# Kernel tuning notes

Measured on AMD Instinct MI355X. Metric: run time of the kernel, lower is better.

Reference implementation:

```python
import jax, jax.numpy as jnp
import numpy as np

P = 113          # vocab (modulus)
D = 128          # residual_dim
H = 4            # n_heads (hardcoded in Model)
DH = D // H      # head_dim = 32
HID = 4 * D      # mlp hidden = 512
BATCH = 131072
RATE = 0.5       # attention_rate


def setup_inputs() -> dict:
    key = jax.random.key(0)
    ks = jax.random.split(key, 12)
    std = 1.0 / D ** 0.5
    x = jax.random.randint(ks[0], (BATCH, 2), 0, P)
    tok_emb = jax.random.normal(ks[1], (P, D), jnp.float32) / D ** 0.5
    pos_emb = jax.random.normal(ks[2], (2, D), jnp.float32) / D ** 0.5
    W_Q = jax.random.normal(ks[3], (H, D, DH), jnp.float32) * std
    W_K = jax.random.normal(ks[4], (H, D, DH), jnp.float32) * std
    W_V = jax.random.normal(ks[5], (H, D, DH), jnp.float32) * std
    W_O = jax.random.normal(ks[6], (H, DH, D), jnp.float32) * std
    # nn.Linear default init: U(-1/sqrt(fan_in), 1/sqrt(fan_in))
    b1_bound = 1.0 / D ** 0.5
    W1 = jax.random.uniform(ks[7], (D, HID), jnp.float32, -b1_bound, b1_bound)
    b1 = jax.random.uniform(ks[8], (HID,), jnp.float32, -b1_bound, b1_bound)
    b2_bound = 1.0 / HID ** 0.5
    W2 = jax.random.uniform(ks[9], (HID, D), jnp.float32, -b2_bound, b2_bound)
    b2 = jax.random.uniform(ks[10], (D,), jnp.float32, -b2_bound, b2_bound)
    W_U = jax.random.normal(ks[11], (P, D), jnp.float32) / P ** 0.5
    return dict(x=x, tok_emb=tok_emb, pos_emb=pos_emb, W_Q=W_Q, W_K=W_K,
                W_V=W_V, W_O=W_O, W1=W1, b1=b1, W2=W2, b2=b2, W_U=W_U)


def reference(x, tok_emb, pos_emb, W_Q, W_K, W_V, W_O, W1, b1, W2, b2, W_U):
    # embed: [B,2,D]
    resid = tok_emb[x] + pos_emb[None, :, :]
    # attention
    q = jnp.einsum('bpd,hdk->bphk', resid, W_Q)
    k = jnp.einsum('bpd,hdk->bphk', resid, W_K)
    v = jnp.einsum('bpd,hdk->bphk', resid, W_V)
    scores = jnp.einsum('bqhk,bshk->bhqs', q, k) / DH ** 0.5  # [B,H,2,2]
    pattern = jax.nn.softmax(scores, axis=-1)
    pattern = (1.0 - RATE) + RATE * pattern  # uniform blend, no causal mask
    z = jnp.einsum('bshk,bhqs->bqhk', v, pattern)
    attn_out = jnp.einsum('bqhk,hkd->bqd', z, W_O)
    resid = resid + attn_out
    # mlp
    h = jax.nn.relu(resid @ W1 + b1)
    resid = resid + (h @ W2 + b2)
    # unembed: [B,2,P]
    logits = jnp.einsum('vd,bpd->bpv', W_U, resid)
    return logits
```

## Files before the change

### kernel.cpp

```cpp
#include <hip/hip_runtime.h>
#include <hip/hip_bf16.h>
#include <stdint.h>

typedef __hip_bfloat16 bf16;
typedef __attribute__((ext_vector_type(8))) short short8;
typedef __attribute__((ext_vector_type(4))) float float4v;

#define NVOCAB 113
#define NPAIR (113 * 113)
#define DDIM 128
#define HIDDIM 512
#define CAP 128
#define LDSB_CAP 1024

#define OFF_B1  145792
#define OFF_B2  211840

#define BOFF_WOT 0
#define BOFF_W1T 16384
#define BOFF_W2T (16384 + 65536)
#define BOFF_WUP (16384 + 65536 + 65536)
#define BTOTAL   (16384 + 65536 + 65536 + 16384)

__device__ __forceinline__ uint16_t f2b(float f) {
  bf16 h = __float2bfloat16(f);
  return *(uint16_t*)&h;
}
__device__ __forceinline__ float b2f(uint16_t u) {
  return __uint_as_float(((uint32_t)u) << 16);
}
__device__ __forceinline__ float ldsrc(const void* p, int i, int isb) {
  return isb ? b2f(((const uint16_t*)p)[i]) : ((const float*)p)[i];
}

struct SrcPtrs { const void* p[11]; };

__global__ void init_kernel(const uint32_t* __restrict__ tok_raw,
                            const uint32_t* __restrict__ x_raw,
                            int* __restrict__ flags,
                            int* __restrict__ cursor) {
  const int idx = blockIdx.x * 256 + threadIdx.x;
  for (int i = idx; i < NPAIR; i += gridDim.x * 256) cursor[i] = 0;
  if (blockIdx.x == 0) {
    __shared__ int cnt_bf16, cnt_xnz;
    if (threadIdx.x == 0) { cnt_bf16 = 0; cnt_xnz = 0; }
    __syncthreads();
    uint32_t u = tok_raw[threadIdx.x];
    int e = (u >> 7) & 0xff;
    if (e >= 100 && e <= 126) atomicAdd(&cnt_bf16, 1);
    uint32_t xv = x_raw[2 * threadIdx.x + 1];
    if (xv != 0u) atomicAdd(&cnt_xnz, 1);
    __syncthreads();
    if (threadIdx.x == 0) {
      flags[0] = (cnt_bf16 >= 128) ? 1 : 0;
      flags[1] = (cnt_xnz == 0) ? 1 : 0;
    }
  }
}

__global__ void __launch_bounds__(384) build_kernel(
    SrcPtrs sp, const uint32_t* __restrict__ x_raw,
    const int* __restrict__ flags, float* __restrict__ wf,
    float* __restrict__ resid_pre, float* __restrict__ qt,
    float* __restrict__ kt, float* __restrict__ vt,
    uint16_t* __restrict__ wb, int* __restrict__ cursor,
    int* __restrict__ blist, int B) {
  const int tid = threadIdx.x;
  const int blk = blockIdx.x;
  const int isb = flags[0];

  if (blk < 226) {
    const int row = blk;
    const int t = row >> 1, p = row & 1;
    __shared__ float r[DDIM];
    if (tid < DDIM) {
      float rv = ldsrc(sp.p[0], t * DDIM + tid, isb) +
                 ldsrc(sp.p[1], p * DDIM + tid, isb);
      r[tid] = rv;
      resid_pre[row * DDIM + tid] = rv;
    }
    __syncthreads();
    const int which = tid >> 7, jj = tid & 127;
    const int h = jj >> 5, j = jj & 31;
    const void* wsrc = sp.p[2 + which];
    const int base = h * 4096 + j;
    float a = 0.f;
    if (isb) {
      const uint16_t* w16 = (const uint16_t*)wsrc;
      #pragma unroll 8
      for (int d = 0; d < 128; ++d)
        a += r[d] * b2f(w16[base + d * 32]);
    } else {
      const float* w32 = (const float*)wsrc;
      #pragma unroll 8
      for (int d = 0; d < 128; ++d)
        a += r[d] * w32[base + d * 32];
    }
    float* outp = (which == 0) ? qt : (which == 1) ? kt : vt;
    outp[row * DDIM + jj] = a;
  } else if (blk < 653) {
    const int idx = (blk - 226) * 384 + tid;
    if (idx < BTOTAL) {
      float v;
      if (idx < BOFF_W1T) {
        int l = idx, d = l >> 7, c = l & 127;
        v = ldsrc(sp.p[5], c * 128 + d, isb);
      } else if (idx < BOFF_W2T) {
        int l = idx - BOFF_W1T, n = l >> 7, d = l & 127;
        v = ldsrc(sp.p[6], d * 512 + n, isb);
      } else if (idx < BOFF_WUP) {
        int l = idx - BOFF_W2T, d = l >> 9, j = l & 511;
        v = ldsrc(sp.p[8], j * 128 + d, isb);
      } else {
        int l = idx - BOFF_WUP, vv = l >> 7, d = l & 127;
        v = (vv < NVOCAB) ? ldsrc(sp.p[10], vv * 128 + d, isb) : 0.f;
      }
      wb[idx] = f2b(v);
    }
  } else if (blk < 655) {
    const int i = (blk - 653) * 384 + tid;
    if (i < 512) wf[OFF_B1 + i] = ldsrc(sp.p[7], i, isb);
    else if (i < 640) wf[OFF_B2 + (i - 512)] = ldsrc(sp.p[9], i - 512, isb);
  } else {
    const int is64 = flags[1];
    const int nthr = (gridDim.x - 655) * 384;
    for (int b = (blk - 655) * 384 + tid; b < B; b += nthr) {
      int t0, t1;
      if (is64) {
        t0 = (int)x_raw[4 * b];
        t1 = (int)x_raw[4 * b + 2];
      } else {
        t0 = (int)x_raw[2 * b];
        t1 = (int)x_raw[2 * b + 1];
      }
      t0 = min(max(t0, 0), NVOCAB - 1);
      t1 = min(max(t1, 0), NVOCAB - 1);
      const int pair = t0 * NVOCAB + t1;
      int pos = atomicAdd(&cursor[pair], 1);
      if (pos < CAP) blist[pair * CAP + pos] = b;
    }
  }
}

__global__ void __launch_bounds__(256, 4) pair_mfma_kernel(
    const float* __restrict__ resid_pre, const float* __restrict__ qt,
    const float* __restrict__ kt, const float* __restrict__ vt,
    const float* __restrict__ wf, const uint16_t* __restrict__ wb,
    const int* __restrict__ cursor, const int* __restrict__ blist,
    float* __restrict__ out) {
  __shared__ uint16_t bufH[16 * 512];
  __shared__ uint16_t bufZ[16 * 128];
  __shared__ uint16_t bufS[16 * 128];
  __shared__ float    spat[8 * 16];
  __shared__ int      smeta[8];
  __shared__ int      ldsb[LDSB_CAP];

  const int tid = threadIdx.x;
  const int blk = blockIdx.x;
  const int lane = tid & 63;
  const int npar = tid >> 6;
  const int l15 = lane & 15, quad = lane >> 4;
  const int mA = l15;

  #define ROW_OF(row_) ({                                        \
    int pr_ = blk * 8 + ((row_) >> 1);                           \
    if (pr_ >= NPAIR) pr_ = NPAIR - 1;                           \
    int t0_ = pr_ / NVOCAB, t1_ = pr_ - t0_ * NVOCAB;            \
    ((row_) & 1) ? t1_ * 2 + 1 : t0_ * 2; })

  if (tid < 8) {
    const int pr = blk * 8 + tid;
    smeta[tid] = (pr < NPAIR) ? min(cursor[pr], CAP) : 0;
  }
  float rpre[2][4];
  #pragma unroll
  for (int ni = 0; ni < 2; ++ni) {
    const int n = (npar + ni * 4) * 16 + l15;
    #pragma unroll
    for (int r = 0; r < 4; ++r)
      rpre[ni][r] = resid_pre[ROW_OF(quad * 4 + r) * DDIM + n];
  }
  float bias1v[8], bias2v[2];
  #pragma unroll
  for (int ni = 0; ni < 8; ++ni)
    bias1v[ni] = wf[OFF_B1 + (npar + ni * 4) * 16 + l15];
  #pragma unroll
  for (int ni = 0; ni < 2; ++ni)
    bias2v[ni] = wf[OFF_B2 + (npar + ni * 4) * 16 + l15];
  const int zm = tid >> 4, zc0 = (tid & 15) * 8;
  float4 zv0a, zv0b, zv1a, zv1b;
  {
    const int zr0 = ROW_OF((zm >> 1) * 2);
    const int zr1 = ROW_OF((zm >> 1) * 2 + 1);
    const float4* p0 = (const float4*)(vt + zr0 * DDIM + zc0);
    const float4* p1 = (const float4*)(vt + zr1 * DDIM + zc0);
    zv0a = p0[0]; zv0b = p0[1]; zv1a = p1[0]; zv1b = p1[1];
  }

  if (tid < 128) {
    const int pl = tid >> 4, s = tid & 15;
    const int pair = blk * 8 + pl;
    if (pair < NPAIR) {
      const int t0 = pair / NVOCAB, t1 = pair - t0 * NVOCAB;
      const int row0 = t0 * 2, row1 = t1 * 2 + 1;
      const int h = s >> 2, qp = (s >> 1) & 1, spp = s & 1;
      const float4* qrow = (const float4*)(qt + (qp ? row1 : row0) * DDIM + h * 32);
      const float4* krow = (const float4*)(kt + (spp ? row1 : row0) * DDIM + h * 32);
      float acc = 0.f;
      #pragma unroll
      for (int j = 0; j < 8; ++j) {
        float4 qv = qrow[j], kv = krow[j];
        acc += qv.x * kv.x + qv.y * kv.y + qv.z * kv.z + qv.w * kv.w;
      }
      spat[pl * 16 + s] = acc * 0.17677669529663687f;
    } else {
      spat[pl * 16 + s] = 0.f;
    }
  }
  __syncthreads();

  int sPre[9];
  sPre[0] = 0;
  #pragma unroll
  for (int q = 0; q < 8; ++q) sPre[q + 1] = sPre[q] + smeta[q];
  const int tot = sPre[8];

  if (tid < 64) {
    const int pl = tid >> 3, s = tid & 7;
    const int base = pl * 16 + s * 2;
    float s0 = spat[base], s1 = spat[base + 1];
    float m = fmaxf(s0, s1);
    float e0 = __expf(s0 - m), e1 = __expf(s1 - m);
    float inv = 1.f / (e0 + e1);
    spat[base]     = 0.5f + 0.5f * e0 * inv;
    spat[base + 1] = 0.5f + 0.5f * e1 * inv;
  } else {
    const int cap = (tot < LDSB_CAP) ? tot : LDSB_CAP;
    for (int i = tid - 64; i < cap; i += 192) {
      int q = 0;
      #pragma unroll
      for (int qq = 1; qq < 8; ++qq)
        if (i >= sPre[qq]) q = qq;
      ldsb[i] = blist[(blk * 8 + q) * CAP + (i - sPre[q])];
    }
  }
  __syncthreads();

  {
    const int pl = zm >> 1, qp = zm & 1;
    const int h = zc0 >> 5;
    const float p0 = spat[pl * 16 + h * 4 + qp * 2];
    const float p1 = spat[pl * 16 + h * 4 + qp * 2 + 1];
    float v0[8] = {zv0a.x, zv0a.y, zv0a.z, zv0a.w, zv0b.x, zv0b.y, zv0b.z, zv0b.w};
    float v1[8] = {zv1a.x, zv1a.y, zv1a.z, zv1a.w, zv1b.x, zv1b.y, zv1b.z, zv1b.w};
    short8 pk;
    #pragma unroll
    for (int e = 0; e < 8; ++e)
      pk[e] = (short)f2b(p0 * v0[e] + p1 * v1[e]);
    *(short8*)&bufZ[(zm * 16 + ((zc0 >> 3) ^ zm)) * 8] = pk;
  }
  __syncthreads();

  float smid[2][4];

  {
    short8 af[4];
    #pragma unroll
    for (int ks = 0; ks < 4; ++ks)
      af[ks] = *(const short8*)&bufZ[(mA * 16 + ((ks * 4 + quad) ^ mA)) * 8];
    short8 bW[2][4];
    #pragma unroll
    for (int ni = 0; ni < 2; ++ni) {
      const int n = (npar + ni * 4) * 16 + l15;
      const uint16_t* bp = wb + BOFF_WOT + n * 128 + quad * 8;
      #pragma unroll
      for (int ks = 0; ks < 4; ++ks)
        bW[ni][ks] = *(const short8*)(bp + ks * 32);
    }
    #pragma unroll
    for (int ni = 0; ni < 2; ++ni) {
      const int n = (npar + ni * 4) * 16 + l15;
      float4v acc = {0.f, 0.f, 0.f, 0.f};
      #pragma unroll
      for (int ks = 0; ks < 4; ++ks)
        acc = __builtin_amdgcn_mfma_f32_16x16x32_bf16(af[ks], bW[ni][ks], acc, 0, 0, 0);
      #pragma unroll
      for (int r = 0; r < 4; ++r) {
        const int row = quad * 4 + r;
        float v = acc[r] + rpre[ni][r];
        smid[ni][r] = v;
        bufS[(row * 16 + ((n >> 3) ^ row)) * 8 + (n & 7)] = f2b(v);
      }
    }
  }
  __syncthreads();

  {
    short8 af[4];
    #pragma unroll
    for (int ks = 0; ks < 4; ++ks)
      af[ks] = *(const short8*)&bufS[(mA * 16 + ((ks * 4 + quad) ^ mA)) * 8];
    #pragma unroll
    for (int half = 0; half < 2; ++half) {
      short8 bW[4][4];
      #pragma unroll
      for (int nj = 0; nj < 4; ++nj) {
        const int ni = half * 4 + nj;
        const int n = (npar + ni * 4) * 16 + l15;
        const uint16_t* bp = wb + BOFF_W1T + n * 128 + quad * 8;
        #pragma unroll
        for (int ks = 0; ks < 4; ++ks)
          bW[nj][ks] = *(const short8*)(bp + ks * 32);
      }
      #pragma unroll
      for (int nj = 0; nj < 4; ++nj) {
        const int ni = half * 4 + nj;
        const int n = (npar + ni * 4) * 16 + l15;
        float4v acc = {0.f, 0.f, 0.f, 0.f};
        #pragma unroll
        for (int ks = 0; ks < 4; ++ks)
          acc = __builtin_amdgcn_mfma_f32_16x16x32_bf16(af[ks], bW[nj][ks], acc, 0, 0, 0);
        const float bias = bias1v[ni];
        #pragma unroll
        for (int r = 0; r < 4; ++r) {
          const int row = quad * 4 + r;
          bufH[(row * 64 + ((n >> 3) ^ row)) * 8 + (n & 7)] =
              f2b(fmaxf(acc[r] + bias, 0.f));
        }
      }
    }
  }
  __syncthreads();

  {
    const int n0 = npar * 16 + l15;
    const int n1 = (npar + 4) * 16 + l15;
    const uint16_t* bp0 = wb + BOFF_W2T + n0 * 512 + quad * 8;
    const uint16_t* bp1 = wb + BOFF_W2T + n1 * 512 + quad * 8;
    float4v acc0 = {0.f, 0.f, 0.f, 0.f};
    float4v acc1 = {0.f, 0.f, 0.f, 0.f};
    #pragma unroll
    for (int half = 0; half < 2; ++half) {
      short8 ah[8], b0[8], b1[8];
      #pragma unroll
      for (int k8 = 0; k8 < 8; ++k8) {
        const int ks = half * 8 + k8;
        ah[k8] = *(const short8*)&bufH[(mA * 64 + ((ks * 4 + quad) ^ mA)) * 8];
        b0[k8] = *(const short8*)(bp0 + ks * 32);
        b1[k8] = *(const short8*)(bp1 + ks * 32);
      }
      #pragma unroll
      for (int k8 = 0; k8 < 8; ++k8) {
        acc0 = __builtin_amdgcn_mfma_f32_16x16x32_bf16(ah[k8], b0[k8], acc0, 0, 0, 0);
        acc1 = __builtin_amdgcn_mfma_f32_16x16x32_bf16(ah[k8], b1[k8], acc1, 0, 0, 0);
      }
    }
    #pragma unroll
    for (int r = 0; r < 4; ++r) {
      const int row = quad * 4 + r;
      bufZ[(row * 16 + ((n0 >> 3) ^ row)) * 8 + (n0 & 7)] =
          f2b(acc0[r] + bias2v[0] + smid[0][r]);
      bufZ[(row * 16 + ((n1 >> 3) ^ row)) * 8 + (n1 & 7)] =
          f2b(acc1[r] + bias2v[1] + smid[1][r]);
    }
  }
  __syncthreads();

  float* lds_log = (float*)bufH;
  {
    short8 ar[4];
    #pragma unroll
    for (int ks = 0; ks < 4; ++ks)
      ar[ks] = *(const short8*)&bufZ[(mA * 16 + ((ks * 4 + quad) ^ mA)) * 8];
    short8 bW[2][4];
    #pragma unroll
    for (int ni = 0; ni < 2; ++ni) {
      const int n = (npar + ni * 4) * 16 + l15;
      const uint16_t* bp = wb + BOFF_WUP + n * 128 + quad * 8;
      #pragma unroll
      for (int ks = 0; ks < 4; ++ks)
        bW[ni][ks] = *(const short8*)(bp + ks * 32);
    }
    #pragma unroll
    for (int ni = 0; ni < 2; ++ni) {
      const int n = (npar + ni * 4) * 16 + l15;
      float4v acc = {0.f, 0.f, 0.f, 0.f};
      #pragma unroll
      for (int ks = 0; ks < 4; ++ks)
        acc = __builtin_amdgcn_mfma_f32_16x16x32_bf16(ar[ks], bW[ni][ks], acc, 0, 0, 0);
      if (n < NVOCAB) {
        #pragma unroll
        for (int r = 0; r < 4; ++r) {
          const int row = quad * 4 + r;
          lds_log[(row >> 1) * 226 + (row & 1) * 113 + n] = acc[r];
        }
      }
    }
  }
  __syncthreads();

  {
    const int wid = tid >> 6;
    const float2* lds2 = (const float2*)lds_log;
    for (int w = wid; w < tot; w += 4) {
      int pl = 0;
      #pragma unroll
      for (int q = 1; q < 8; ++q)
        if (w >= sPre[q]) pl = q;
      const int b = (w < LDSB_CAP) ? ldsb[w]
                                   : blist[(blk * 8 + pl) * CAP + (w - sPre[pl])];
      const float2* src = lds2 + pl * 113;
      float2* dst = (float2*)out + (size_t)b * 113;
      dst[lane] = src[lane];
      const int j2 = lane + 64;
      if (j2 < 113) dst[j2] = src[j2];
    }
  }
  #undef ROW_OF
}

extern "C" void kernel_launch(void* const* d_in, const int* in_sizes, int n_in,
                              void* d_out, int out_size, void* d_ws, size_t ws_size,
                              hipStream_t stream) {
  int*      flags     = (int*)d_ws;
  float*    wf        = (float*)((char*)d_ws + 256);
  float*    resid_pre = (float*)((char*)d_ws + 905984);
  float*    qt        = (float*)((char*)d_ws + 1021696);
  float*    kt        = (float*)((char*)d_ws + 1137408);
  float*    vt        = (float*)((char*)d_ws + 1253120);
  int*      cursor    = (int*)((char*)d_ws + 1368832);
  int*      blist     = (int*)((char*)d_ws + 1420288);
  uint16_t* wb        = (uint16_t*)((char*)d_ws + 12912016);

  const int B = in_sizes[0] / 2;

  init_kernel<<<64, 256, 0, stream>>>((const uint32_t*)d_in[1],
                                      (const uint32_t*)d_in[0], flags, cursor);

  SrcPtrs sp;
  for (int i = 0; i < 11; ++i) sp.p[i] = d_in[i + 1];

  build_kernel<<<997, 384, 0, stream>>>(
      sp, (const uint32_t*)d_in[0], flags, wf, resid_pre, qt, kt, vt, wb,
      cursor, blist, B);

  const int nblk = (NPAIR + 7) / 8;
  pair_mfma_kernel<<<nblk, 256, 0, stream>>>(resid_pre, qt, kt, vt, wf, wb,
                                             cursor, blist, (float*)d_out);
}
```

Baseline: 232.9 us.

## Double pairs per block and reuse weight fragments across two M tiles

```diff
diff --git a/kernel.cpp b/kernel.cpp
--- a/kernel.cpp
+++ b/kernel.cpp
@@ -5,13 +5,16 @@
 typedef __hip_bfloat16 bf16;
 typedef __attribute__((ext_vector_type(8))) short short8;
 typedef __attribute__((ext_vector_type(4))) float float4v;
+typedef __attribute__((ext_vector_type(2))) float float2v;
 
 #define NVOCAB 113
 #define NPAIR (113 * 113)
 #define DDIM 128
 #define HIDDIM 512
 #define CAP 128
-#define LDSB_CAP 1024
+#define PAIRS_PB 16
+#define ROWS_PB 32
+#define LDSB_CAP 512
 
 #define OFF_B1  145792
 #define OFF_B2  211840
@@ -142,17 +145,17 @@
   }
 }
 
-__global__ void __launch_bounds__(256, 4) pair_mfma_kernel(
+__global__ void __launch_bounds__(512, 3) pair_mfma_kernel(
     const float* __restrict__ resid_pre, const float* __restrict__ qt,
     const float* __restrict__ kt, const float* __restrict__ vt,
     const float* __restrict__ wf, const uint16_t* __restrict__ wb,
     const int* __restrict__ cursor, const int* __restrict__ blist,
     float* __restrict__ out) {
-  __shared__ uint16_t bufH[16 * 512];
-  __shared__ uint16_t bufZ[16 * 128];
-  __shared__ uint16_t bufS[16 * 128];
-  __shared__ float    spat[8 * 16];
-  __shared__ int      smeta[8];
+  __shared__ uint16_t bufH[ROWS_PB * 512];
+  __shared__ uint16_t bufZ[ROWS_PB * 128];
+  __shared__ uint16_t bufS[ROWS_PB * 128];
+  __shared__ float    spat[PAIRS_PB * 16];
+  __shared__ int      smeta[PAIRS_PB];
   __shared__ int      ldsb[LDSB_CAP];
 
   const int tid = threadIdx.x;
@@ -160,33 +163,29 @@
   const int lane = tid & 63;
   const int npar = tid >> 6;
   const int l15 = lane & 15, quad = lane >> 4;
-  const int mA = l15;
 
   #define ROW_OF(row_) ({                                        \
-    int pr_ = blk * 8 + ((row_) >> 1);                           \
+    int pr_ = blk * PAIRS_PB + ((row_) >> 1);                    \
     if (pr_ >= NPAIR) pr_ = NPAIR - 1;                           \
     int t0_ = pr_ / NVOCAB, t1_ = pr_ - t0_ * NVOCAB;            \
     ((row_) & 1) ? t1_ * 2 + 1 : t0_ * 2; })
 
-  if (tid < 8) {
-    const int pr = blk * 8 + tid;
+  if (tid < PAIRS_PB) {
+    const int pr = blk * PAIRS_PB + tid;
     smeta[tid] = (pr < NPAIR) ? min(cursor[pr], CAP) : 0;
   }
+  const int nG = npar * 16 + l15;
   float rpre[2][4];
   #pragma unroll
-  for (int ni = 0; ni < 2; ++ni) {
-    const int n = (npar + ni * 4) * 16 + l15;
+  for (int mf = 0; mf < 2; ++mf)
     #pragma unroll
     for (int r = 0; r < 4; ++r)
-      rpre[ni][r] = resid_pre[ROW_OF(quad * 4 + r) * DDIM + n];
-  }
-  float bias1v[8], bias2v[2];
+      rpre[mf][r] = resid_pre[ROW_OF(mf * 16 + quad * 4 + r) * DDIM + nG];
+  float bias1v[4];
   #pragma unroll
-  for (int ni = 0; ni < 8; ++ni)
-    bias1v[ni] = wf[OFF_B1 + (npar + ni * 4) * 16 + l15];
-  #pragma unroll
-  for (int ni = 0; ni < 2; ++ni)
-    bias2v[ni] = wf[OFF_B2 + (npar + ni * 4) * 16 + l15];
+  for (int ni = 0; ni < 4; ++ni)
+    bias1v[ni] = wf[OFF_B1 + (npar + ni * 8) * 16 + l15];
+  const float bias2 = wf[OFF_B2 + nG];
   const int zm = tid >> 4, zc0 = (tid & 15) * 8;
   float4 zv0a, zv0b, zv1a, zv1b;
   {
@@ -197,9 +196,9 @@
     zv0a = p0[0]; zv0b = p0[1]; zv1a = p1[0]; zv1b = p1[1];
   }
 
-  if (tid < 128) {
+  if (tid < 256) {
     const int pl = tid >> 4, s = tid & 15;
-    const int pair = blk * 8 + pl;
+    const int pair = blk * PAIRS_PB + pl;
     if (pair < NPAIR) {
       const int t0 = pair / NVOCAB, t1 = pair - t0 * NVOCAB;
       const int row0 = t0 * 2, row1 = t1 * 2 + 1;
@@ -219,13 +218,13 @@
   }
   __syncthreads();
 
-  int sPre[9];
+  int sPre[PAIRS_PB + 1];
   sPre[0] = 0;
   #pragma unroll
-  for (int q = 0; q < 8; ++q) sPre[q + 1] = sPre[q] + smeta[q];
-  const int tot = sPre[8];
-
-  if (tid < 64) {
+  for (int q = 0; q < PAIRS_PB; ++q) sPre[q + 1] = sPre[q] + smeta[q];
+  const int tot = sPre[PAIRS_PB];
+
+  if (tid < 128) {
     const int pl = tid >> 3, s = tid & 7;
     const int base = pl * 16 + s * 2;
     float s0 = spat[base], s1 = spat[base + 1];
@@ -235,13 +234,13 @@
     spat[base]     = 0.5f + 0.5f * e0 * inv;
     spat[base + 1] = 0.5f + 0.5f * e1 * inv;
   } else {
-    const int cap = (tot < LDSB_CAP) ? tot : LDSB_CAP;
-    for (int i = tid - 64; i < cap; i += 192) {
+    const int cap2 = (tot < LDSB_CAP) ? tot : LDSB_CAP;
+    for (int i = tid - 128; i < cap2; i += 384) {
       int q = 0;
       #pragma unroll
-      for (int qq = 1; qq < 8; ++qq)
+      for (int qq = 1; qq < PAIRS_PB; ++qq)
         if (i >= sPre[qq]) q = qq;
-      ldsb[i] = blist[(blk * 8 + q) * CAP + (i - sPre[q])];
+      ldsb[i] = blist[(blk * PAIRS_PB + q) * CAP + (i - sPre[q])];
     }
   }
   __syncthreads();
@@ -257,163 +256,184 @@
     #pragma unroll
     for (int e = 0; e < 8; ++e)
       pk[e] = (short)f2b(p0 * v0[e] + p1 * v1[e]);
-    *(short8*)&bufZ[(zm * 16 + ((zc0 >> 3) ^ zm)) * 8] = pk;
+    *(short8*)&bufZ[(zm * 16 + ((zc0 >> 3) ^ (zm & 15))) * 8] = pk;
   }
   __syncthreads();
 
   float smid[2][4];
 
   {
-    short8 af[4];
-    #pragma unroll
-    for (int ks = 0; ks < 4; ++ks)
-      af[ks] = *(const short8*)&bufZ[(mA * 16 + ((ks * 4 + quad) ^ mA)) * 8];
-    short8 bW[2][4];
-    #pragma unroll
-    for (int ni = 0; ni < 2; ++ni) {
-      const int n = (npar + ni * 4) * 16 + l15;
-      const uint16_t* bp = wb + BOFF_WOT + n * 128 + quad * 8;
-      #pragma unroll
-      for (int ks = 0; ks < 4; ++ks)
-        bW[ni][ks] = *(const short8*)(bp + ks * 32);
-    }
-    #pragma unroll
-    for (int ni = 0; ni < 2; ++ni) {
-      const int n = (npar + ni * 4) * 16 + l15;
-      float4v acc = {0.f, 0.f, 0.f, 0.f};
-      #pragma unroll
-      for (int ks = 0; ks < 4; ++ks)
-        acc = __builtin_amdgcn_mfma_f32_16x16x32_bf16(af[ks], bW[ni][ks], acc, 0, 0, 0);
+    short8 af[2][4];
+    #pragma unroll
+    for (int mf = 0; mf < 2; ++mf)
+      #pragma unroll
+      for (int ks = 0; ks < 4; ++ks)
+        af[mf][ks] = *(const short8*)&bufZ[((mf * 16 + l15) * 16 +
+                                           ((ks * 4 + quad) ^ l15)) * 8];
+    short8 bW[4];
+    {
+      const uint16_t* bp = wb + BOFF_WOT + nG * 128 + quad * 8;
+      #pragma unroll
+      for (int ks = 0; ks < 4; ++ks)
+        bW[ks] = *(const short8*)(bp + ks * 32);
+    }
+    float4v acc[2] = {{0.f, 0.f, 0.f, 0.f}, {0.f, 0.f, 0.f, 0.f}};
+    #pragma unroll
+    for (int mf = 0; mf < 2; ++mf)
+      #pragma unroll
+      for (int ks = 0; ks < 4; ++ks)
+        acc[mf] = __builtin_amdgcn_mfma_f32_16x16x32_bf16(af[mf][ks], bW[ks],
+                                                          acc[mf], 0, 0, 0);
+    #pragma unroll
+    for (int mf = 0; mf < 2; ++mf)
       #pragma unroll
       for (int r = 0; r < 4; ++r) {
-        const int row = quad * 4 + r;
-        float v = acc[r] + rpre[ni][r];
-        smid[ni][r] = v;
-        bufS[(row * 16 + ((n >> 3) ^ row)) * 8 + (n & 7)] = f2b(v);
-      }
-    }
-  }
-  __syncthreads();
-
-  {
-    short8 af[4];
-    #pragma unroll
-    for (int ks = 0; ks < 4; ++ks)
-      af[ks] = *(const short8*)&bufS[(mA * 16 + ((ks * 4 + quad) ^ mA)) * 8];
+        const int row = mf * 16 + quad * 4 + r;
+        float v = acc[mf][r] + rpre[mf][r];
+        smid[mf][r] = v;
+        bufS[(row * 16 + ((nG >> 3) ^ (row & 15))) * 8 + (nG & 7)] = f2b(v);
+      }
+  }
+  __syncthreads();
+
+  {
+    short8 af[2][4];
+    #pragma unroll
+    for (int mf = 0; mf < 2; ++mf)
+      #pragma unroll
+      for (int ks = 0; ks < 4; ++ks)
+        af[mf][ks] = *(const short8*)&bufS[((mf * 16 + l15) * 16 +
+                                           ((ks * 4 + quad) ^ l15)) * 8];
     #pragma unroll
     for (int half = 0; half < 2; ++half) {
-      short8 bW[4][4];
-      #pragma unroll
-      for (int nj = 0; nj < 4; ++nj) {
-        const int ni = half * 4 + nj;
-        const int n = (npar + ni * 4) * 16 + l15;
+      short8 bW[2][4];
+      #pragma unroll
+      for (int nj = 0; nj < 2; ++nj) {
+        const int ni = half * 2 + nj;
+        const int n = (npar + ni * 8) * 16 + l15;
         const uint16_t* bp = wb + BOFF_W1T + n * 128 + quad * 8;
         #pragma unroll
         for (int ks = 0; ks < 4; ++ks)
           bW[nj][ks] = *(const short8*)(bp + ks * 32);
       }
       #pragma unroll
-      for (int nj = 0; nj < 4; ++nj) {
-        const int ni = half * 4 + nj;
-        const int n = (npar + ni * 4) * 16 + l15;
-        float4v acc = {0.f, 0.f, 0.f, 0.f};
-        #pragma unroll
-        for (int ks = 0; ks < 4; ++ks)
-          acc = __builtin_amdgcn_mfma_f32_16x16x32_bf16(af[ks], bW[nj][ks], acc, 0, 0, 0);
+      for (int nj = 0; nj < 2; ++nj) {
+        const int ni = half * 2 + nj;
+        const int n = (npar + ni * 8) * 16 + l15;
+        float4v acc[2] = {{0.f, 0.f, 0.f, 0.f}, {0.f, 0.f, 0.f, 0.f}};
+        #pragma unroll
+        for (int mf = 0; mf < 2; ++mf)
+          #pragma unroll
+          for (int ks = 0; ks < 4; ++ks)
+            acc[mf] = __builtin_amdgcn_mfma_f32_16x16x32_bf16(
+                af[mf][ks], bW[nj][ks], acc[mf], 0, 0, 0);
         const float bias = bias1v[ni];
         #pragma unroll
-        for (int r = 0; r < 4; ++r) {
-          const int row = quad * 4 + r;
-          bufH[(row * 64 + ((n >> 3) ^ row)) * 8 + (n & 7)] =
-              f2b(fmaxf(acc[r] + bias, 0.f));
-        }
-      }
-    }
-  }
-  __syncthreads();
-
-  {
-    const int n0 = npar * 16 + l15;
-    const int n1 = (npar + 4) * 16 + l15;
-    const uint16_t* bp0 = wb + BOFF_W2T + n0 * 512 + quad * 8;
-    const uint16_t* bp1 = wb + BOFF_W2T + n1 * 512 + quad * 8;
+        for (int mf = 0; mf < 2; ++mf)
+          #pragma unroll
+          for (int r = 0; r < 4; ++r) {
+            const int row = mf * 16 + quad * 4 + r;
+            bufH[(row * 64 + ((n >> 3) ^ (row & 15))) * 8 + (n & 7)] =
+                f2b(fmaxf(acc[mf][r] + bias, 0.f));
+          }
+      }
+    }
+  }
+  __syncthreads();
+
+  {
+    const uint16_t* bp = wb + BOFF_W2T + nG * 512 + quad * 8;
     float4v acc0 = {0.f, 0.f, 0.f, 0.f};
     float4v acc1 = {0.f, 0.f, 0.f, 0.f};
     #pragma unroll
     for (int half = 0; half < 2; ++half) {
-      short8 ah[8], b0[8], b1[8];
-      #pragma unroll
-      for (int k8 = 0; k8 < 8; ++k8) {
-        const int ks = half * 8 + k8;
-        ah[k8] = *(const short8*)&bufH[(mA * 64 + ((ks * 4 + quad) ^ mA)) * 8];
-        b0[k8] = *(const short8*)(bp0 + ks * 32);
-        b1[k8] = *(const short8*)(bp1 + ks * 32);
-      }
-      #pragma unroll
-      for (int k8 = 0; k8 < 8; ++k8) {
-        acc0 = __builtin_amdgcn_mfma_f32_16x16x32_bf16(ah[k8], b0[k8], acc0, 0, 0, 0);
-        acc1 = __builtin_amdgcn_mfma_f32_16x16x32_bf16(ah[k8], b1[k8], acc1, 0, 0, 0);
+      short8 bB[8];
+      #pragma unroll
+      for (int k8 = 0; k8 < 8; ++k8)
+        bB[k8] = *(const short8*)(bp + (half * 8 + k8) * 32);
+      #pragma unroll
+      for (int qtr = 0; qtr < 2; ++qtr) {
+        short8 a0[4], a1[4];
+        #pragma unroll
+        for (int k4 = 0; k4 < 4; ++k4) {
+          const int ks = half * 8 + qtr * 4 + k4;
+          a0[k4] = *(const short8*)&bufH[(l15 * 64 +
+                                         ((ks * 4 + quad) ^ l15)) * 8];
+          a1[k4] = *(const short8*)&bufH[((16 + l15) * 64 +
+                                         ((ks * 4 + quad) ^ l15)) * 8];
+        }
+        #pragma unroll
+        for (int k4 = 0; k4 < 4; ++k4) {
+          acc0 = __builtin_amdgcn_mfma_f32_16x16x32_bf16(
+              a0[k4], bB[qtr * 4 + k4], acc0, 0, 0, 0);
+          acc1 = __builtin_amdgcn_mfma_f32_16x16x32_bf16(
+              a1[k4], bB[qtr * 4 + k4], acc1, 0, 0, 0);
+        }
       }
     }
     #pragma unroll
     for (int r = 0; r < 4; ++r) {
-      const int row = quad * 4 + r;
-      bufZ[(row * 16 + ((n0 >> 3) ^ row)) * 8 + (n0 & 7)] =
-          f2b(acc0[r] + bias2v[0] + smid[0][r]);
-      bufZ[(row * 16 + ((n1 >> 3) ^ row)) * 8 + (n1 & 7)] =
-          f2b(acc1[r] + bias2v[1] + smid[1][r]);
+      const int row0 = quad * 4 + r;
+      const int row1 = 16 + quad * 4 + r;
+      bufZ[(row0 * 16 + ((nG >> 3) ^ (row0 & 15))) * 8 + (nG & 7)] =
+          f2b(acc0[r] + bias2 + smid[0][r]);
+      bufZ[(row1 * 16 + ((nG >> 3) ^ (row1 & 15))) * 8 + (nG & 7)] =
+          f2b(acc1[r] + bias2 + smid[1][r]);
     }
   }
   __syncthreads();
 
   float* lds_log = (float*)bufH;
   {
-    short8 ar[4];
-    #pragma unroll
-    for (int ks = 0; ks < 4; ++ks)
-      ar[ks] = *(const short8*)&bufZ[(mA * 16 + ((ks * 4 + quad) ^ mA)) * 8];
-    short8 bW[2][4];
-    #pragma unroll
-    for (int ni = 0; ni < 2; ++ni) {
-      const int n = (npar + ni * 4) * 16 + l15;
-      const uint16_t* bp = wb + BOFF_WUP + n * 128 + quad * 8;
-      #pragma unroll
-      for (int ks = 0; ks < 4; ++ks)
-        bW[ni][ks] = *(const short8*)(bp + ks * 32);
-    }
-    #pragma unroll
-    for (int ni = 0; ni < 2; ++ni) {
-      const int n = (npar + ni * 4) * 16 + l15;
-      float4v acc = {0.f, 0.f, 0.f, 0.f};
-      #pragma unroll
-      for (int ks = 0; ks < 4; ++ks)
-        acc = __builtin_amdgcn_mfma_f32_16x16x32_bf16(ar[ks], bW[ni][ks], acc, 0, 0, 0);
-      if (n < NVOCAB) {
+    short8 ar[2][4];
+    #pragma unroll
+    for (int mf = 0; mf < 2; ++mf)
+      #pragma unroll
+      for (int ks = 0; ks < 4; ++ks)
+        ar[mf][ks] = *(const short8*)&bufZ[((mf * 16 + l15) * 16 +
+                                           ((ks * 4 + quad) ^ l15)) * 8];
+    short8 bW[4];
+    {
+      const uint16_t* bp = wb + BOFF_WUP + nG * 128 + quad * 8;
+      #pragma unroll
+      for (int ks = 0; ks < 4; ++ks)
+        bW[ks] = *(const short8*)(bp + ks * 32);
+    }
+    float4v acc[2] = {{0.f, 0.f, 0.f, 0.f}, {0.f, 0.f, 0.f, 0.f}};
+    #pragma unroll
+    for (int mf = 0; mf < 2; ++mf)
+      #pragma unroll
+      for (int ks = 0; ks < 4; ++ks)
+        acc[mf] = __builtin_amdgcn_mfma_f32_16x16x32_bf16(ar[mf][ks], bW[ks],
+                                                          acc[mf], 0, 0, 0);
+    if (nG < NVOCAB) {
+      #pragma unroll
+      for (int mf = 0; mf < 2; ++mf)
         #pragma unroll
         for (int r = 0; r < 4; ++r) {
-          const int row = quad * 4 + r;
-          lds_log[(row >> 1) * 226 + (row & 1) * 113 + n] = acc[r];
+          const int row = mf * 16 + quad * 4 + r;
+          lds_log[(row >> 1) * 226 + (row & 1) * 113 + nG] = acc[mf][r];
         }
-      }
     }
   }
   __syncthreads();
 
   {
     const int wid = tid >> 6;
-    const float2* lds2 = (const float2*)lds_log;
-    for (int w = wid; w < tot; w += 4) {
+    const float2v* lds2 = (const float2v*)lds_log;
+    for (int w = wid; w < tot; w += 8) {
       int pl = 0;
       #pragma unroll
-      for (int q = 1; q < 8; ++q)
+      for (int q = 1; q < PAIRS_PB; ++q)
         if (w >= sPre[q]) pl = q;
-      const int b = (w < LDSB_CAP) ? ldsb[w]
-                                   : blist[(blk * 8 + pl) * CAP + (w - sPre[pl])];
-      const float2* src = lds2 + pl * 113;
-      float2* dst = (float2*)out + (size_t)b * 113;
-      dst[lane] = src[lane];
+      const int b = (w < LDSB_CAP)
+                        ? ldsb[w]
+                        : blist[(blk * PAIRS_PB + pl) * CAP + (w - sPre[pl])];
+      const float2v* src = lds2 + pl * 113;
+      float2v* dst = (float2v*)out + (size_t)b * 113;
+      __builtin_nontemporal_store(src[lane], dst + lane);
       const int j2 = lane + 64;
-      if (j2 < 113) dst[j2] = src[j2];
+      if (j2 < 113) __builtin_nontemporal_store(src[j2], dst + j2);
     }
   }
   #undef ROW_OF
@@ -444,7 +464,7 @@
       sp, (const uint32_t*)d_in[0], flags, wf, resid_pre, qt, kt, vt, wb,
       cursor, blist, B);
 
-  const int nblk = (NPAIR + 7) / 8;
-  pair_mfma_kernel<<<nblk, 256, 0, stream>>>(resid_pre, qt, kt, vt, wf, wb,
+  const int nblk = (NPAIR + PAIRS_PB - 1) / PAIRS_PB;
+  pair_mfma_kernel<<<nblk, 512, 0, stream>>>(resid_pre, qt, kt, vt, wf, wb,
                                              cursor, blist, (float*)d_out);
 }
```

After: 234.4 us. Within noise of the previous version (+0.6%).
